# Kernel optimization log

Hardware: AMD Instinct MI355X
Metric: run time of the kernel (lower is better)

The kernel has to match this reference:

```python
import jax, jax.numpy as jnp
import numpy as np
import math

B, S, HID, NH, HD = 2, 1024, 768, 12, 64
MAXP = 1024  # max_position_embeddings


def setup_inputs() -> dict:
    key = jax.random.key(0)
    ks = jax.random.split(key, 12)
    s = 0.02
    return {
        "hidden_states": jax.random.normal(ks[0], (B, S, HID), jnp.float32),
        "attention_mask": jnp.zeros((B, 1, 1, S), jnp.float32),
        "scaled_attention_mask": jax.random.uniform(ks[1], (1, 1, S, S), dtype=jnp.float32),
        "selector_outputs": jax.random.uniform(ks[2], (B, 1, S, 1), dtype=jnp.float32),
        "Wq": jax.random.normal(ks[3], (HID, HID), jnp.float32) * s,
        "bq": jnp.zeros((HID,), jnp.float32),
        "Wk": jax.random.normal(ks[4], (HID, HID), jnp.float32) * s,
        "bk": jnp.zeros((HID,), jnp.float32),
        "Wv": jax.random.normal(ks[5], (HID, HID), jnp.float32) * s,
        "bv": jnp.zeros((HID,), jnp.float32),
        "dist_emb": jax.random.normal(ks[6], (2 * MAXP - 1, HD), jnp.float32) * s,
    }


def _heads(x):
    # [B,S,HID] -> [B,NH,S,HD]
    return x.reshape(B, S, NH, HD).transpose(0, 2, 1, 3)


def reference(hidden_states, attention_mask, scaled_attention_mask, selector_outputs,
              Wq, bq, Wk, bk, Wv, bv, dist_emb):
    q = _heads(hidden_states @ Wq + bq)  # [B,NH,S,HD]
    k = _heads(hidden_states @ Wk + bk)
    v = _heads(hidden_states @ Wv + bv)

    scores = jnp.einsum('bhld,bhrd->bhlr', q, k)  # [B,NH,S,S]

    # relative_key positional bias
    pos = jnp.arange(S)
    dist_idx = pos[:, None] - pos[None, :] + (MAXP - 1)  # [S,S] in [0, 2*MAXP-2]
    pos_emb = dist_emb[dist_idx]  # [S,S,HD]
    scores = scores + jnp.einsum('bhld,lrd->bhlr', q, pos_emb)

    scores = scores / math.sqrt(HD)
    scores = scores + attention_mask  # additive mask (global branch)

    probs = jax.nn.softmax(scores, axis=-1)  # dropout prob = 0.0 -> identity
    context = jnp.einsum('bhlr,bhrd->bhld', probs, v)

    # local (selector-gated) branch; note: attention_mask added a second time,
    # faithful to the original code
    scores_l = scores * scaled_attention_mask + attention_mask
    probs_l = jax.nn.softmax(scores_l, axis=-1)
    local_context = jnp.einsum('bhlr,bhrd->bhld', probs_l, v)

    sel = selector_outputs  # [B,1,S,1]
    context = sel * local_context + (1.0 - sel) * context  # [B,NH,S,HD]

    # [B,NH,S,HD] -> [B,S,HID]
    return context.transpose(0, 2, 1, 3).reshape(B, S, HID)
```

## Files before the change

kernel.cpp:

```cpp
#include <hip/hip_runtime.h>
#include <hip/hip_bf16.h>
#include <math.h>

#define BB   2
#define SS   1024
#define HIDD 768
#define NHH  12
#define HDD  64

typedef float f32x4 __attribute__((ext_vector_type(4)));
typedef short bf8   __attribute__((ext_vector_type(8)));
typedef unsigned short u16;
typedef unsigned int u32;
typedef u16 u16x8 __attribute__((ext_vector_type(8)));
typedef u16 u16x4 __attribute__((ext_vector_type(4)));

__device__ __forceinline__ u16 f2bf(float x) {
  unsigned int u = __float_as_uint(x);
  u += 0x7fffu + ((u >> 16) & 1u);
  return (u16)(u >> 16);
}
__device__ __forceinline__ float bf2f(u16 x) {
  return __uint_as_float(((u32)x) << 16);
}

__device__ __forceinline__ bf8 ldfrag(const u16* t, int row, int kc) {
  return *(const bf8*)&t[row * 64 + (kc ^ ((row & 7) << 3))];
}

__global__ __launch_bounds__(256) void xconv_kernel(const float* __restrict__ X,
                                                    u16* __restrict__ Xb) {
  int i = (blockIdx.x * 256 + threadIdx.x) * 8;
  float4 a = *(const float4*)&X[i];
  float4 b = *(const float4*)&X[i + 4];
  u16x8 o;
  o[0] = f2bf(a.x); o[1] = f2bf(a.y); o[2] = f2bf(a.z); o[3] = f2bf(a.w);
  o[4] = f2bf(b.x); o[5] = f2bf(b.y); o[6] = f2bf(b.z); o[7] = f2bf(b.w);
  *(u16x8*)&Xb[i] = o;
}

__global__ __launch_bounds__(256) void wtconv_kernel(
    const float* __restrict__ Wq, const float* __restrict__ Wk,
    const float* __restrict__ Wv, u16* __restrict__ Wt) {
  const int zi = blockIdx.z;
  const float* __restrict__ W = (zi == 0) ? Wq : (zi == 1 ? Wk : Wv);
  const int n0 = blockIdx.x * 64;
  const int k0 = blockIdx.y * 64;
  __shared__ float t[64][65];
  const int tid = threadIdx.x;
  {
    const int kl = tid >> 4;
    const int nl = (tid & 15) * 4;
#pragma unroll
    for (int p = 0; p < 4; ++p) {
      float4 v = *(const float4*)&W[(size_t)(k0 + kl + 16 * p) * HIDD + n0 + nl];
      t[kl + 16 * p][nl + 0] = v.x;
      t[kl + 16 * p][nl + 1] = v.y;
      t[kl + 16 * p][nl + 2] = v.z;
      t[kl + 16 * p][nl + 3] = v.w;
    }
  }
  __syncthreads();
  {
    const int nl = tid >> 4;
    const int cl = (tid & 15) * 4;
#pragma unroll
    for (int p = 0; p < 4; ++p) {
      const int n = nl + 16 * p;
      u16x4 o;
      o[0] = f2bf(t[cl + 0][n]);
      o[1] = f2bf(t[cl + 1][n]);
      o[2] = f2bf(t[cl + 2][n]);
      o[3] = f2bf(t[cl + 3][n]);
      *(u16x4*)&Wt[(size_t)(zi * HIDD + n0 + n) * HIDD + k0 + cl] = o;
    }
  }
}

__global__ __launch_bounds__(256) void econv_kernel(const float* __restrict__ demb,
                                                    u16* __restrict__ eb) {
  int i = (blockIdx.x * 256 + threadIdx.x) * 8;
  if (i < 2047 * HDD) {
    float4 a = *(const float4*)&demb[i];
    float4 b = *(const float4*)&demb[i + 4];
    u16x8 o;
    o[0] = f2bf(a.x); o[1] = f2bf(a.y); o[2] = f2bf(a.z); o[3] = f2bf(a.w);
    o[4] = f2bf(b.x); o[5] = f2bf(b.y); o[6] = f2bf(b.z); o[7] = f2bf(b.w);
    *(u16x8*)&eb[i] = o;
  }
}

__global__ __launch_bounds__(256) void qkv_mfma_kernel(
    const u16* __restrict__ Xb,
    const u16* __restrict__ Wt,
    const float* __restrict__ bq, const float* __restrict__ bk,
    const float* __restrict__ bv,
    u16* __restrict__ qb, u16* __restrict__ kb, u16* __restrict__ vt) {
  const int bn = blockIdx.x;
  const int bm = blockIdx.y;
  const int zi = bn / 6;

  __shared__ u16 As[64 * 64];
  __shared__ u16 Bs[128 * 64];

  const int tid  = threadIdx.x;
  const int lane = tid & 63;
  const int w    = tid >> 6;
  const int g    = lane >> 4;
  const int ln   = lane & 15;
  const int wm   = (w >> 1) * 32;
  const int wn   = (w & 1) * 64;

  f32x4 acc[2][4] = {};

  const int srow = tid >> 3;
  const int scol = (tid & 7) * 8;
  const u16* Ag = Xb + (size_t)(bm * 64 + srow) * HIDD + scol;
  const u16* Bg = Wt + (size_t)(bn * 128 + srow) * HIDD + scol;

  for (int k0 = 0; k0 < HIDD; k0 += 64) {
    if (k0) __syncthreads();
#pragma unroll
    for (int p = 0; p < 2; ++p) {
      const int r = srow + 32 * p;
      const int sw = (r & 7) << 3;
      *(u16x8*)&As[r * 64 + (scol ^ sw)] =
          *(const u16x8*)&Ag[(size_t)(32 * p) * HIDD + k0];
    }
#pragma unroll
    for (int p = 0; p < 4; ++p) {
      const int r = srow + 32 * p;
      const int sw = (r & 7) << 3;
      *(u16x8*)&Bs[r * 64 + (scol ^ sw)] =
          *(const u16x8*)&Bg[(size_t)(32 * p) * HIDD + k0];
    }
    __syncthreads();

    bf8 af[2][2], bfr[4][2];
#pragma unroll
    for (int f = 0; f < 2; ++f)
#pragma unroll
      for (int kk = 0; kk < 2; ++kk)
        af[f][kk] = ldfrag(As, wm + 16 * f + ln, kk * 32 + g * 8);
#pragma unroll
    for (int f = 0; f < 4; ++f)
#pragma unroll
      for (int kk = 0; kk < 2; ++kk)
        bfr[f][kk] = ldfrag(Bs, wn + 16 * f + ln, kk * 32 + g * 8);
    if (zi < 2) {
#pragma unroll
      for (int mf = 0; mf < 2; ++mf)
#pragma unroll
        for (int nf = 0; nf < 4; ++nf)
#pragma unroll
          for (int kk = 0; kk < 2; ++kk)
            acc[mf][nf] = __builtin_amdgcn_mfma_f32_16x16x32_bf16(
                bfr[nf][kk], af[mf][kk], acc[mf][nf], 0, 0, 0);
    } else {
#pragma unroll
      for (int mf = 0; mf < 2; ++mf)
#pragma unroll
        for (int nf = 0; nf < 4; ++nf)
#pragma unroll
          for (int kk = 0; kk < 2; ++kk)
            acc[mf][nf] = __builtin_amdgcn_mfma_f32_16x16x32_bf16(
                af[mf][kk], bfr[nf][kk], acc[mf][nf], 0, 0, 0);
    }
  }

  const int mrow  = bm * 64 + wm;
  const int nbase = (bn % 6) * 128 + wn;
  const int h     = nbase >> 6;

  if (zi < 2) {
    const float* __restrict__ bias = zi ? bk : bq;
    u16* __restrict__ outp = zi ? kb : qb;
#pragma unroll
    for (int nf = 0; nf < 4; ++nf) {
      const int d0 = 16 * nf + 4 * g;
      float4 bi = *(const float4*)&bias[nbase + d0];
#pragma unroll
      for (int mf = 0; mf < 2; ++mf) {
        const int m = mrow + 16 * mf + ln;
        const int b = m >> 10, s = m & 1023;
        u16x4 o;
        o[0] = f2bf(acc[mf][nf][0] + bi.x);
        o[1] = f2bf(acc[mf][nf][1] + bi.y);
        o[2] = f2bf(acc[mf][nf][2] + bi.z);
        o[3] = f2bf(acc[mf][nf][3] + bi.w);
        *(u16x4*)&outp[(((size_t)(b * NHH + h)) * SS + s) * HDD + d0] = o;
      }
    }
  } else {
#pragma unroll
    for (int nf = 0; nf < 4; ++nf) {
      const int d = 16 * nf + ln;
      const float bi = bv[nbase + d];
#pragma unroll
      for (int mf = 0; mf < 2; ++mf) {
        const int m = mrow + 16 * mf + 4 * g;
        const int b = m >> 10, s = m & 1023;
        u16x4 o;
        o[0] = f2bf(acc[mf][nf][0] + bi);
        o[1] = f2bf(acc[mf][nf][1] + bi);
        o[2] = f2bf(acc[mf][nf][2] + bi);
        o[3] = f2bf(acc[mf][nf][3] + bi);
        *(u16x4*)&vt[(((size_t)(b * NHH + h)) * HDD + d) * SS + s] = o;
      }
    }
  }
}

__global__ __launch_bounds__(256, 3) void attn_kernel(
    const u16* __restrict__ qbg,
    const u16* __restrict__ kbg,
    const u16* __restrict__ vtg,
    const u16* __restrict__ eb,
    const float* __restrict__ am,
    const float* __restrict__ smask,
    const float* __restrict__ selp,
    float* __restrict__ out) {
  const int l0 = blockIdx.x * 32;
  const int h  = blockIdx.y;
  const int b  = blockIdx.z;
  const int bh = b * NHH + h;
  const size_t hoff = (size_t)bh * SS * HDD;

  __shared__ __align__(16) u16 smbuf[16384];
  __shared__ __align__(4)  u16 tbuf[4 * 80 * 17];

  const int tid  = threadIdx.x;
  const int lane = tid & 63;
  const int w    = tid >> 6;
  const int p    = w >> 1;
  const int wp   = w & 1;
  const int g    = lane >> 4;
  const int ln   = lane & 15;

  u16* ksw = smbuf + p * 4096;
  u16* vsw = smbuf + 8192 + p * 4096;
  u16* Tw  = tbuf + w * (80 * 17);

  bf8 qf[2];
  {
    const u16* qp = qbg + hoff + (size_t)(l0 + 16 * wp + ln) * HDD + g * 8;
    qf[0] = *(const bf8*)(qp);
    qf[1] = *(const bf8*)(qp + 32);
  }

  f32x4 acc1[4] = {}, acc2[4] = {};
  float m1 = -INFINITY, m2 = -INFINITY, sum1 = 0.f, sum2 = 0.f;

  const int tid128 = tid & 127;
  const int rr = tid128 >> 2;
  const int cc = (tid128 & 3) << 4;
  const int S0i = ((lane & 16) << 1) | ln;
  const int S1i = S0i + 16;
  const bool ghi = (lane & 32) != 0;

  for (int t = 0; t < 8; ++t) {
    const int r0 = 512 * p + 64 * t;
    __syncthreads();

    const int W0 = l0 + 16 * wp - r0 + 960;
    bf8 ef[5][2];
#pragma unroll
    for (int c5 = 0; c5 < 5; ++c5) {
      const int gr = min(W0 + 16 * c5 + ln, 2046);
      const u16* ep = eb + (size_t)gr * HDD + g * 8;
      ef[c5][0] = *(const bf8*)(ep);
      ef[c5][1] = *(const bf8*)(ep + 32);
    }
    f32x4 amv[4], smv[4];
#pragma unroll
    for (int ct = 0; ct < 4; ++ct) {
      amv[ct] = *(const f32x4*)&am[(b << 10) + r0 + 16 * ct + 4 * g];
      smv[ct] = *(const f32x4*)&smask[(size_t)(l0 + 16 * wp + ln) * SS +
                                      r0 + 16 * ct + 4 * g];
    }
    {
      const u16* kgp = kbg + hoff + (size_t)r0 * HDD;
      const u16* vgp = vtg + hoff + r0;
#pragma unroll
      for (int pp = 0; pp < 2; ++pp) {
        const int r = rr + 32 * pp;
        const int sw = (r & 7) << 3;
        u16x8 a0 = *(const u16x8*)&kgp[(size_t)r * HDD + cc];
        u16x8 a1 = *(const u16x8*)&kgp[(size_t)r * HDD + cc + 8];
        *(u16x8*)&ksw[r * 64 + (cc ^ sw)] = a0;
        *(u16x8*)&ksw[r * 64 + ((cc + 8) ^ sw)] = a1;
        u16x8 c0 = *(const u16x8*)&vgp[(size_t)r * SS + cc];
        u16x8 c1 = *(const u16x8*)&vgp[(size_t)r * SS + cc + 8];
        *(u16x8*)&vsw[r * 64 + (cc ^ sw)] = c0;
        *(u16x8*)&vsw[r * 64 + ((cc + 8) ^ sw)] = c1;
      }
    }
    __syncthreads();

    __builtin_amdgcn_s_setprio(1);
#pragma unroll
    for (int c5 = 0; c5 < 5; ++c5) {
      f32x4 x = {0.f, 0.f, 0.f, 0.f};
      x = __builtin_amdgcn_mfma_f32_16x16x32_bf16(ef[c5][0], qf[0], x, 0, 0, 0);
      x = __builtin_amdgcn_mfma_f32_16x16x32_bf16(ef[c5][1], qf[1], x, 0, 0, 0);
#pragma unroll
      for (int i = 0; i < 4; ++i)
        Tw[(16 * c5 + 4 * g + i) * 17 + ln] = f2bf(x[i]);
    }
    f32x4 sc[4];
#pragma unroll
    for (int ct = 0; ct < 4; ++ct) {
      f32x4 x = {0.f, 0.f, 0.f, 0.f};
#pragma unroll
      for (int kk = 0; kk < 2; ++kk)
        x = __builtin_amdgcn_mfma_f32_16x16x32_bf16(
            ldfrag(ksw, ct * 16 + ln, kk * 32 + g * 8), qf[kk], x, 0, 0, 0);
      sc[ct] = x;
    }
    __builtin_amdgcn_s_setprio(0);

    float s1r[4][4], s2r[4][4];
#pragma unroll
    for (int ct = 0; ct < 4; ++ct)
#pragma unroll
      for (int i = 0; i < 4; ++i) {
        const int e = ln + 63 - 16 * ct - 4 * g - i;
        const float tb = bf2f(Tw[e * 17 + ln]);
        const float s1 = (sc[ct][i] + tb) * 0.125f + amv[ct][i];
        s1r[ct][i] = s1;
        s2r[ct][i] = s1 * smv[ct][i] + amv[ct][i];
      }

    bf8 pa1[2], pa2[2];
    {
      float mx = s1r[0][0];
#pragma unroll
      for (int ct = 0; ct < 4; ++ct)
#pragma unroll
        for (int i = 0; i < 4; ++i) mx = fmaxf(mx, s1r[ct][i]);
      mx = fmaxf(mx, __shfl_xor(mx, 16, 64));
      mx = fmaxf(mx, __shfl_xor(mx, 32, 64));
      const float mn = fmaxf(m1, mx);
      const float scl = __expf(m1 - mn);
      m1 = mn;
      float rs = 0.f;
      u32 pk[4][2];
#pragma unroll
      for (int ct = 0; ct < 4; ++ct) {
        const float p0 = __expf(s1r[ct][0] - mn);
        const float p1 = __expf(s1r[ct][1] - mn);
        const float p2 = __expf(s1r[ct][2] - mn);
        const float p3 = __expf(s1r[ct][3] - mn);
        rs += (p0 + p1) + (p2 + p3);
        pk[ct][0] = (u32)f2bf(p0) | ((u32)f2bf(p1) << 16);
        pk[ct][1] = (u32)f2bf(p2) | ((u32)f2bf(p3) << 16);
      }
      rs += __shfl_xor(rs, 16, 64);
      rs += __shfl_xor(rs, 32, 64);
      sum1 = sum1 * scl + rs;
#pragma unroll
      for (int i = 0; i < 4; ++i) {
        const float s = __shfl(scl, (lane & 48) + 4 * g + i, 64);
#pragma unroll
        for (int dt = 0; dt < 4; ++dt) acc1[dt][i] *= s;
      }
#pragma unroll
      for (int kk = 0; kk < 2; ++kk) {
        union { u32 u[4]; bf8 v; } f;
        const int cA = 2 * kk, cB = 2 * kk + 1;
        u32 a, bb;
        a = (u32)__shfl((int)pk[cA][0], S0i, 64);
        bb = (u32)__shfl((int)pk[cB][0], S0i, 64);
        f.u[0] = ghi ? bb : a;
        a = (u32)__shfl((int)pk[cA][1], S0i, 64);
        bb = (u32)__shfl((int)pk[cB][1], S0i, 64);
        f.u[1] = ghi ? bb : a;
        a = (u32)__shfl((int)pk[cA][0], S1i, 64);
        bb = (u32)__shfl((int)pk[cB][0], S1i, 64);
        f.u[2] = ghi ? bb : a;
        a = (u32)__shfl((int)pk[cA][1], S1i, 64);
        bb = (u32)__shfl((int)pk[cB][1], S1i, 64);
        f.u[3] = ghi ? bb : a;
        pa1[kk] = f.v;
      }
    }
    {
      float mx = s2r[0][0];
#pragma unroll
      for (int ct = 0; ct < 4; ++ct)
#pragma unroll
        for (int i = 0; i < 4; ++i) mx = fmaxf(mx, s2r[ct][i]);
      mx = fmaxf(mx, __shfl_xor(mx, 16, 64));
      mx = fmaxf(mx, __shfl_xor(mx, 32, 64));
      const float mn = fmaxf(m2, mx);
      const float scl = __expf(m2 - mn);
      m2 = mn;
      float rs = 0.f;
      u32 pk[4][2];
#pragma unroll
      for (int ct = 0; ct < 4; ++ct) {
        const float p0 = __expf(s2r[ct][0] - mn);
        const float p1 = __expf(s2r[ct][1] - mn);
        const float p2 = __expf(s2r[ct][2] - mn);
        const float p3 = __expf(s2r[ct][3] - mn);
        rs += (p0 + p1) + (p2 + p3);
        pk[ct][0] = (u32)f2bf(p0) | ((u32)f2bf(p1) << 16);
        pk[ct][1] = (u32)f2bf(p2) | ((u32)f2bf(p3) << 16);
      }
      rs += __shfl_xor(rs, 16, 64);
      rs += __shfl_xor(rs, 32, 64);
      sum2 = sum2 * scl + rs;
#pragma unroll
      for (int i = 0; i < 4; ++i) {
        const float s = __shfl(scl, (lane & 48) + 4 * g + i, 64);
#pragma unroll
        for (int dt = 0; dt < 4; ++dt) acc2[dt][i] *= s;
      }
#pragma unroll
      for (int kk = 0; kk < 2; ++kk) {
        union { u32 u[4]; bf8 v; } f;
        const int cA = 2 * kk, cB = 2 * kk + 1;
        u32 a, bb;
        a = (u32)__shfl((int)pk[cA][0], S0i, 64);
        bb = (u32)__shfl((int)pk[cB][0], S0i, 64);
        f.u[0] = ghi ? bb : a;
        a = (u32)__shfl((int)pk[cA][1], S0i, 64);
        bb = (u32)__shfl((int)pk[cB][1], S0i, 64);
        f.u[1] = ghi ? bb : a;
        a = (u32)__shfl((int)pk[cA][0], S1i, 64);
        bb = (u32)__shfl((int)pk[cB][0], S1i, 64);
        f.u[2] = ghi ? bb : a;
        a = (u32)__shfl((int)pk[cA][1], S1i, 64);
        bb = (u32)__shfl((int)pk[cB][1], S1i, 64);
        f.u[3] = ghi ? bb : a;
        pa2[kk] = f.v;
      }
    }

    __builtin_amdgcn_s_setprio(1);
#pragma unroll
    for (int kk = 0; kk < 2; ++kk) {
#pragma unroll
      for (int dt = 0; dt < 4; ++dt) {
        bf8 vb = ldfrag(vsw, dt * 16 + ln, kk * 32 + g * 8);
        acc1[dt] = __builtin_amdgcn_mfma_f32_16x16x32_bf16(pa1[kk], vb, acc1[dt], 0, 0, 0);
        acc2[dt] = __builtin_amdgcn_mfma_f32_16x16x32_bf16(pa2[kk], vb, acc2[dt], 0, 0, 0);
      }
    }
    __builtin_amdgcn_s_setprio(0);
  }

  __syncthreads();
  float* scr = (float*)smbuf;
  if (p == 1) {
#pragma unroll
    for (int i = 0; i < 4; ++i) {
      const int row = 4 * g + i;
#pragma unroll
      for (int dt = 0; dt < 4; ++dt) {
        scr[wp * 1024 + row * 64 + dt * 16 + ln] = acc1[dt][i];
        scr[2048 + wp * 1024 + row * 64 + dt * 16 + ln] = acc2[dt][i];
      }
    }
    if (g == 0) {
      const int sb = 4096 + (wp * 16 + ln) * 4;
      scr[sb + 0] = m1;
      scr[sb + 1] = sum1;
      scr[sb + 2] = m2;
      scr[sb + 3] = sum2;
    }
  }
  __syncthreads();
  if (p == 0) {
    const int sb = 4096 + (wp * 16 + ln) * 4;
    const float mB1 = scr[sb + 0], sB1 = scr[sb + 1];
    const float mB2 = scr[sb + 2], sB2 = scr[sb + 3];
    const float M1 = fmaxf(m1, mB1);
    const float e1A = __expf(m1 - M1), e1B = __expf(mB1 - M1);
    const float inv1 = 1.f / (sum1 * e1A + sB1 * e1B);
    const float a1 = e1A * inv1, c1 = e1B * inv1;
    const float M2 = fmaxf(m2, mB2);
    const float e2A = __expf(m2 - M2), e2B = __expf(mB2 - M2);
    const float inv2 = 1.f / (sum2 * e2A + sB2 * e2B);
    const float a2 = e2A * inv2, c2 = e2B * inv2;
#pragma unroll
    for (int i = 0; i < 4; ++i) {
      const int src = (lane & 48) + 4 * g + i;
      const float a1s = __shfl(a1, src, 64), c1s = __shfl(c1, src, 64);
      const float a2s = __shfl(a2, src, 64), c2s = __shfl(c2, src, 64);
      const int row = 4 * g + i;
      const int lg = l0 + 16 * wp + row;
      const float se = selp[(b << 10) + lg];
#pragma unroll
      for (int dt = 0; dt < 4; ++dt) {
        const float aB1 = scr[wp * 1024 + row * 64 + dt * 16 + ln];
        const float aB2 = scr[2048 + wp * 1024 + row * 64 + dt * 16 + ln];
        const float o1 = acc1[dt][i] * a1s + aB1 * c1s;
        const float o2 = acc2[dt][i] * a2s + aB2 * c2s;
        out[((size_t)((b << 10) + lg)) * HIDD + h * HDD + dt * 16 + ln] =
            se * o2 + (1.f - se) * o1;
      }
    }
  }
}

extern "C" void kernel_launch(void* const* d_in, const int* in_sizes, int n_in,
                              void* d_out, int out_size, void* d_ws, size_t ws_size,
                              hipStream_t stream) {
  const float* hidden = (const float*)d_in[0];
  const float* am     = (const float*)d_in[1];
  const float* smask  = (const float*)d_in[2];
  const float* selp   = (const float*)d_in[3];
  const float* Wq     = (const float*)d_in[4];
  const float* bq     = (const float*)d_in[5];
  const float* Wk     = (const float*)d_in[6];
  const float* bk     = (const float*)d_in[7];
  const float* Wv     = (const float*)d_in[8];
  const float* bv     = (const float*)d_in[9];
  const float* demb   = (const float*)d_in[10];
  float* out = (float*)d_out;

  u16* wsp = (u16*)d_ws;
  const size_t NEL = (size_t)BB * NHH * SS * HDD;
  u16* Xb  = wsp;
  u16* Wt  = Xb + (size_t)2048 * HIDD;
  u16* qbw = Wt + (size_t)3 * HIDD * HIDD;
  u16* kbw = qbw + NEL;
  u16* vtw = kbw + NEL;
  u16* ebw = vtw + NEL;

  xconv_kernel<<<768, 256, 0, stream>>>(hidden, Xb);
  dim3 gw(HIDD / 64, HIDD / 64, 3);
  wtconv_kernel<<<gw, 256, 0, stream>>>(Wq, Wk, Wv, Wt);
  econv_kernel<<<64, 256, 0, stream>>>(demb, ebw);

  dim3 g1(18, 32);
  qkv_mfma_kernel<<<g1, 256, 0, stream>>>(Xb, Wt, bq, bk, bv, qbw, kbw, vtw);

  dim3 g2(SS / 32, NHH, BB);
  attn_kernel<<<g2, 256, 0, stream>>>(qbw, kbw, vtw, ebw, am, smask, selp, out);
}
```

Before: 102.0 us.

## Load K/V fragments directly from global memory, drop LDS staging, remap blocks per XCD

New measurement: 138.7 us. 36.0% more time.

```diff
diff --git a/kernel.cpp b/kernel.cpp
--- a/kernel.cpp
+++ b/kernel.cpp
@@ -211,7 +211,7 @@
   }
 }
 
-__global__ __launch_bounds__(256, 3) void attn_kernel(
+__global__ __launch_bounds__(128, 3) void attn_kernel(
     const u16* __restrict__ qbg,
     const u16* __restrict__ kbg,
     const u16* __restrict__ vtg,
@@ -220,30 +220,33 @@
     const float* __restrict__ smask,
     const float* __restrict__ selp,
     float* __restrict__ out) {
-  const int l0 = blockIdx.x * 32;
-  const int h  = blockIdx.y;
-  const int b  = blockIdx.z;
+  const int d    = blockIdx.x;
+  const int xcd  = d & 7;
+  const int qq   = d >> 3;
+  const int inner = qq & 63;
+  const int grp  = qq >> 6;
+  const int hg   = grp * 8 + xcd;
+  const int h    = hg % NHH;
+  const int b    = hg / NHH;
+  const int l0   = inner * 16;
+
   const int bh = b * NHH + h;
   const size_t hoff = (size_t)bh * SS * HDD;
 
-  __shared__ __align__(16) u16 smbuf[16384];
-  __shared__ __align__(4)  u16 tbuf[4 * 80 * 17];
+  __shared__ __align__(4)  u16  tbuf[2 * 80 * 20];
+  __shared__ __align__(16) float scr[2112];
 
   const int tid  = threadIdx.x;
   const int lane = tid & 63;
   const int w    = tid >> 6;
-  const int p    = w >> 1;
-  const int wp   = w & 1;
   const int g    = lane >> 4;
   const int ln   = lane & 15;
 
-  u16* ksw = smbuf + p * 4096;
-  u16* vsw = smbuf + 8192 + p * 4096;
-  u16* Tw  = tbuf + w * (80 * 17);
+  u16* Tw = tbuf + w * (80 * 20);
 
   bf8 qf[2];
   {
-    const u16* qp = qbg + hoff + (size_t)(l0 + 16 * wp + ln) * HDD + g * 8;
+    const u16* qp = qbg + hoff + (size_t)(l0 + ln) * HDD + g * 8;
     qf[0] = *(const bf8*)(qp);
     qf[1] = *(const bf8*)(qp + 32);
   }
@@ -251,18 +254,21 @@
   f32x4 acc1[4] = {}, acc2[4] = {};
   float m1 = -INFINITY, m2 = -INFINITY, sum1 = 0.f, sum2 = 0.f;
 
-  const int tid128 = tid & 127;
-  const int rr = tid128 >> 2;
-  const int cc = (tid128 & 3) << 4;
   const int S0i = ((lane & 16) << 1) | ln;
   const int S1i = S0i + 16;
   const bool ghi = (lane & 32) != 0;
 
   for (int t = 0; t < 8; ++t) {
-    const int r0 = 512 * p + 64 * t;
-    __syncthreads();
-
-    const int W0 = l0 + 16 * wp - r0 + 960;
+    const int r0 = 512 * w + 64 * t;
+
+    bf8 kf[4][2];
+#pragma unroll
+    for (int ct = 0; ct < 4; ++ct) {
+      const u16* kp = kbg + hoff + (size_t)(r0 + 16 * ct + ln) * HDD + g * 8;
+      kf[ct][0] = *(const bf8*)(kp);
+      kf[ct][1] = *(const bf8*)(kp + 32);
+    }
+    const int W0 = l0 - r0 + 960;
     bf8 ef[5][2];
 #pragma unroll
     for (int c5 = 0; c5 < 5; ++c5) {
@@ -275,27 +281,8 @@
 #pragma unroll
     for (int ct = 0; ct < 4; ++ct) {
       amv[ct] = *(const f32x4*)&am[(b << 10) + r0 + 16 * ct + 4 * g];
-      smv[ct] = *(const f32x4*)&smask[(size_t)(l0 + 16 * wp + ln) * SS +
-                                      r0 + 16 * ct + 4 * g];
-    }
-    {
-      const u16* kgp = kbg + hoff + (size_t)r0 * HDD;
-      const u16* vgp = vtg + hoff + r0;
-#pragma unroll
-      for (int pp = 0; pp < 2; ++pp) {
-        const int r = rr + 32 * pp;
-        const int sw = (r & 7) << 3;
-        u16x8 a0 = *(const u16x8*)&kgp[(size_t)r * HDD + cc];
-        u16x8 a1 = *(const u16x8*)&kgp[(size_t)r * HDD + cc + 8];
-        *(u16x8*)&ksw[r * 64 + (cc ^ sw)] = a0;
-        *(u16x8*)&ksw[r * 64 + ((cc + 8) ^ sw)] = a1;
-        u16x8 c0 = *(const u16x8*)&vgp[(size_t)r * SS + cc];
-        u16x8 c1 = *(const u16x8*)&vgp[(size_t)r * SS + cc + 8];
-        *(u16x8*)&vsw[r * 64 + (cc ^ sw)] = c0;
-        *(u16x8*)&vsw[r * 64 + ((cc + 8) ^ sw)] = c1;
-      }
-    }
-    __syncthreads();
+      smv[ct] = *(const f32x4*)&smask[(size_t)(l0 + ln) * SS + r0 + 16 * ct + 4 * g];
+    }
 
     __builtin_amdgcn_s_setprio(1);
 #pragma unroll
@@ -305,16 +292,14 @@
       x = __builtin_amdgcn_mfma_f32_16x16x32_bf16(ef[c5][1], qf[1], x, 0, 0, 0);
 #pragma unroll
       for (int i = 0; i < 4; ++i)
-        Tw[(16 * c5 + 4 * g + i) * 17 + ln] = f2bf(x[i]);
+        Tw[(16 * c5 + 4 * g + i) * 20 + ln] = f2bf(x[i]);
     }
     f32x4 sc[4];
 #pragma unroll
     for (int ct = 0; ct < 4; ++ct) {
       f32x4 x = {0.f, 0.f, 0.f, 0.f};
-#pragma unroll
-      for (int kk = 0; kk < 2; ++kk)
-        x = __builtin_amdgcn_mfma_f32_16x16x32_bf16(
-            ldfrag(ksw, ct * 16 + ln, kk * 32 + g * 8), qf[kk], x, 0, 0, 0);
+      x = __builtin_amdgcn_mfma_f32_16x16x32_bf16(kf[ct][0], qf[0], x, 0, 0, 0);
+      x = __builtin_amdgcn_mfma_f32_16x16x32_bf16(kf[ct][1], qf[1], x, 0, 0, 0);
       sc[ct] = x;
     }
     __builtin_amdgcn_s_setprio(0);
@@ -325,7 +310,7 @@
 #pragma unroll
       for (int i = 0; i < 4; ++i) {
         const int e = ln + 63 - 16 * ct - 4 * g - i;
-        const float tb = bf2f(Tw[e * 17 + ln]);
+        const float tb = bf2f(Tw[e * 20 + ln]);
         const float s1 = (sc[ct][i] + tb) * 0.125f + amv[ct][i];
         s1r[ct][i] = s1;
         s2r[ct][i] = s1 * smv[ct][i] + amv[ct][i];
@@ -442,7 +427,8 @@
     for (int kk = 0; kk < 2; ++kk) {
 #pragma unroll
       for (int dt = 0; dt < 4; ++dt) {
-        bf8 vb = ldfrag(vsw, dt * 16 + ln, kk * 32 + g * 8);
+        const bf8 vb = *(const bf8*)(vtg + hoff + (size_t)(16 * dt + ln) * SS +
+                                     r0 + kk * 32 + g * 8);
         acc1[dt] = __builtin_amdgcn_mfma_f32_16x16x32_bf16(pa1[kk], vb, acc1[dt], 0, 0, 0);
         acc2[dt] = __builtin_amdgcn_mfma_f32_16x16x32_bf16(pa2[kk], vb, acc2[dt], 0, 0, 0);
       }
@@ -451,19 +437,18 @@
   }
 
   __syncthreads();
-  float* scr = (float*)smbuf;
-  if (p == 1) {
+  if (w == 1) {
 #pragma unroll
     for (int i = 0; i < 4; ++i) {
       const int row = 4 * g + i;
 #pragma unroll
       for (int dt = 0; dt < 4; ++dt) {
-        scr[wp * 1024 + row * 64 + dt * 16 + ln] = acc1[dt][i];
-        scr[2048 + wp * 1024 + row * 64 + dt * 16 + ln] = acc2[dt][i];
+        scr[row * 64 + dt * 16 + ln] = acc1[dt][i];
+        scr[1024 + row * 64 + dt * 16 + ln] = acc2[dt][i];
       }
     }
     if (g == 0) {
-      const int sb = 4096 + (wp * 16 + ln) * 4;
+      const int sb = 2048 + ln * 4;
       scr[sb + 0] = m1;
       scr[sb + 1] = sum1;
       scr[sb + 2] = m2;
@@ -471,8 +456,8 @@
     }
   }
   __syncthreads();
-  if (p == 0) {
-    const int sb = 4096 + (wp * 16 + ln) * 4;
+  if (w == 0) {
+    const int sb = 2048 + ln * 4;
     const float mB1 = scr[sb + 0], sB1 = scr[sb + 1];
     const float mB2 = scr[sb + 2], sB2 = scr[sb + 3];
     const float M1 = fmaxf(m1, mB1);
@@ -489,12 +474,12 @@
       const float a1s = __shfl(a1, src, 64), c1s = __shfl(c1, src, 64);
       const float a2s = __shfl(a2, src, 64), c2s = __shfl(c2, src, 64);
       const int row = 4 * g + i;
-      const int lg = l0 + 16 * wp + row;
+      const int lg = l0 + row;
       const float se = selp[(b << 10) + lg];
 #pragma unroll
       for (int dt = 0; dt < 4; ++dt) {
-        const float aB1 = scr[wp * 1024 + row * 64 + dt * 16 + ln];
-        const float aB2 = scr[2048 + wp * 1024 + row * 64 + dt * 16 + ln];
+        const float aB1 = scr[row * 64 + dt * 16 + ln];
+        const float aB2 = scr[1024 + row * 64 + dt * 16 + ln];
         const float o1 = acc1[dt][i] * a1s + aB1 * c1s;
         const float o2 = acc2[dt][i] * a2s + aB2 * c2s;
         out[((size_t)((b << 10) + lg)) * HIDD + h * HDD + dt * 16 + ln] =
@@ -537,6 +522,5 @@
   dim3 g1(18, 32);
   qkv_mfma_kernel<<<g1, 256, 0, stream>>>(Xb, Wt, bq, bk, bv, qbw, kbw, vtw);
 
-  dim3 g2(SS / 32, NHH, BB);
-  attn_kernel<<<g2, 256, 0, stream>>>(qbw, kbw, vtw, ebw, am, smask, selp, out);
-}
+  attn_kernel<<<1536, 128, 0, stream>>>(qbw, kbw, vtw, ebw, am, smask, selp, out);
+}
```

## Prefetch K/V tiles into registers, bf16 scaled mask, XCD-aware block remap

Applied to the files above, without the earlier changes.

Result: slower. 105.5 us (+3.5%).

```diff
diff --git a/kernel.cpp b/kernel.cpp
--- a/kernel.cpp
+++ b/kernel.cpp
@@ -90,6 +90,17 @@
   }
 }
 
+__global__ __launch_bounds__(256) void sconv_kernel(const float* __restrict__ sm,
+                                                    u16* __restrict__ smb) {
+  int i = (blockIdx.x * 256 + threadIdx.x) * 8;
+  float4 a = *(const float4*)&sm[i];
+  float4 b = *(const float4*)&sm[i + 4];
+  u16x8 o;
+  o[0] = f2bf(a.x); o[1] = f2bf(a.y); o[2] = f2bf(a.z); o[3] = f2bf(a.w);
+  o[4] = f2bf(b.x); o[5] = f2bf(b.y); o[6] = f2bf(b.z); o[7] = f2bf(b.w);
+  *(u16x8*)&smb[i] = o;
+}
+
 __global__ __launch_bounds__(256) void qkv_mfma_kernel(
     const u16* __restrict__ Xb,
     const u16* __restrict__ Wt,
@@ -217,17 +228,24 @@
     const u16* __restrict__ vtg,
     const u16* __restrict__ eb,
     const float* __restrict__ am,
-    const float* __restrict__ smask,
+    const u16* __restrict__ smb,
     const float* __restrict__ selp,
     float* __restrict__ out) {
-  const int l0 = blockIdx.x * 32;
-  const int h  = blockIdx.y;
-  const int b  = blockIdx.z;
+  const int bid  = blockIdx.x;
+  const int xcd  = bid & 7;
+  const int idx  = bid >> 3;
+  const int inner = idx & 31;
+  const int grp  = idx >> 5;
+  const int hg   = grp * 8 + xcd;
+  const int h    = hg % NHH;
+  const int b    = hg / NHH;
+  const int l0   = inner * 32;
+
   const int bh = b * NHH + h;
   const size_t hoff = (size_t)bh * SS * HDD;
 
   __shared__ __align__(16) u16 smbuf[16384];
-  __shared__ __align__(4)  u16 tbuf[4 * 80 * 17];
+  __shared__ __align__(4)  u16 tbuf[4 * 80 * 20];
 
   const int tid  = threadIdx.x;
   const int lane = tid & 63;
@@ -239,7 +257,7 @@
 
   u16* ksw = smbuf + p * 4096;
   u16* vsw = smbuf + 8192 + p * 4096;
-  u16* Tw  = tbuf + w * (80 * 17);
+  u16* Tw  = tbuf + w * (80 * 20);
 
   bf8 qf[2];
   {
@@ -258,9 +276,24 @@
   const int S1i = S0i + 16;
   const bool ghi = (lane & 32) != 0;
 
+  const u16* kgp0 = kbg + hoff;
+  const u16* vgp0 = vtg + hoff;
+
+  u16x8 kr[2][2], vr[2][2];
+  {
+    const int r0 = 512 * p;
+#pragma unroll
+    for (int pp = 0; pp < 2; ++pp) {
+      const int r = rr + 32 * pp;
+      kr[pp][0] = *(const u16x8*)&kgp0[(size_t)(r0 + r) * HDD + cc];
+      kr[pp][1] = *(const u16x8*)&kgp0[(size_t)(r0 + r) * HDD + cc + 8];
+      vr[pp][0] = *(const u16x8*)&vgp0[(size_t)r * SS + r0 + cc];
+      vr[pp][1] = *(const u16x8*)&vgp0[(size_t)r * SS + r0 + cc + 8];
+    }
+  }
+
   for (int t = 0; t < 8; ++t) {
     const int r0 = 512 * p + 64 * t;
-    __syncthreads();
 
     const int W0 = l0 + 16 * wp - r0 + 960;
     bf8 ef[5][2];
@@ -271,31 +304,38 @@
       ef[c5][0] = *(const bf8*)(ep);
       ef[c5][1] = *(const bf8*)(ep + 32);
     }
-    f32x4 amv[4], smv[4];
+    f32x4 amv[4];
+    u16x4 smv[4];
 #pragma unroll
     for (int ct = 0; ct < 4; ++ct) {
       amv[ct] = *(const f32x4*)&am[(b << 10) + r0 + 16 * ct + 4 * g];
-      smv[ct] = *(const f32x4*)&smask[(size_t)(l0 + 16 * wp + ln) * SS +
-                                      r0 + 16 * ct + 4 * g];
-    }
-    {
-      const u16* kgp = kbg + hoff + (size_t)r0 * HDD;
-      const u16* vgp = vtg + hoff + r0;
+      smv[ct] = *(const u16x4*)&smb[(size_t)(l0 + 16 * wp + ln) * SS +
+                                    r0 + 16 * ct + 4 * g];
+    }
+
+    __syncthreads();
+#pragma unroll
+    for (int pp = 0; pp < 2; ++pp) {
+      const int r = rr + 32 * pp;
+      const int sw = (r & 7) << 3;
+      *(u16x8*)&ksw[r * 64 + (cc ^ sw)] = kr[pp][0];
+      *(u16x8*)&ksw[r * 64 + ((cc + 8) ^ sw)] = kr[pp][1];
+      *(u16x8*)&vsw[r * 64 + (cc ^ sw)] = vr[pp][0];
+      *(u16x8*)&vsw[r * 64 + ((cc + 8) ^ sw)] = vr[pp][1];
+    }
+    __syncthreads();
+
+    if (t < 7) {
+      const int rn = r0 + 64;
 #pragma unroll
       for (int pp = 0; pp < 2; ++pp) {
         const int r = rr + 32 * pp;
-        const int sw = (r & 7) << 3;
-        u16x8 a0 = *(const u16x8*)&kgp[(size_t)r * HDD + cc];
-        u16x8 a1 = *(const u16x8*)&kgp[(size_t)r * HDD + cc + 8];
-        *(u16x8*)&ksw[r * 64 + (cc ^ sw)] = a0;
-        *(u16x8*)&ksw[r * 64 + ((cc + 8) ^ sw)] = a1;
-        u16x8 c0 = *(const u16x8*)&vgp[(size_t)r * SS + cc];
-        u16x8 c1 = *(const u16x8*)&vgp[(size_t)r * SS + cc + 8];
-        *(u16x8*)&vsw[r * 64 + (cc ^ sw)] = c0;
-        *(u16x8*)&vsw[r * 64 + ((cc + 8) ^ sw)] = c1;
-      }
-    }
-    __syncthreads();
+        kr[pp][0] = *(const u16x8*)&kgp0[(size_t)(rn + r) * HDD + cc];
+        kr[pp][1] = *(const u16x8*)&kgp0[(size_t)(rn + r) * HDD + cc + 8];
+        vr[pp][0] = *(const u16x8*)&vgp0[(size_t)r * SS + rn + cc];
+        vr[pp][1] = *(const u16x8*)&vgp0[(size_t)r * SS + rn + cc + 8];
+      }
+    }
 
     __builtin_amdgcn_s_setprio(1);
 #pragma unroll
@@ -305,7 +345,7 @@
       x = __builtin_amdgcn_mfma_f32_16x16x32_bf16(ef[c5][1], qf[1], x, 0, 0, 0);
 #pragma unroll
       for (int i = 0; i < 4; ++i)
-        Tw[(16 * c5 + 4 * g + i) * 17 + ln] = f2bf(x[i]);
+        Tw[(16 * c5 + 4 * g + i) * 20 + ln] = f2bf(x[i]);
     }
     f32x4 sc[4];
 #pragma unroll
@@ -325,10 +365,10 @@
 #pragma unroll
       for (int i = 0; i < 4; ++i) {
         const int e = ln + 63 - 16 * ct - 4 * g - i;
-        const float tb = bf2f(Tw[e * 17 + ln]);
+        const float tb = bf2f(Tw[e * 20 + ln]);
         const float s1 = (sc[ct][i] + tb) * 0.125f + amv[ct][i];
         s1r[ct][i] = s1;
-        s2r[ct][i] = s1 * smv[ct][i] + amv[ct][i];
+        s2r[ct][i] = s1 * bf2f(smv[ct][i]) + amv[ct][i];
       }
 
     bf8 pa1[2], pa2[2];
@@ -528,15 +568,16 @@
   u16* kbw = qbw + NEL;
   u16* vtw = kbw + NEL;
   u16* ebw = vtw + NEL;
+  u16* smb = ebw + (size_t)2047 * HDD;
 
   xconv_kernel<<<768, 256, 0, stream>>>(hidden, Xb);
   dim3 gw(HIDD / 64, HIDD / 64, 3);
   wtconv_kernel<<<gw, 256, 0, stream>>>(Wq, Wk, Wv, Wt);
   econv_kernel<<<64, 256, 0, stream>>>(demb, ebw);
+  sconv_kernel<<<512, 256, 0, stream>>>(smask, smb);
 
   dim3 g1(18, 32);
   qkv_mfma_kernel<<<g1, 256, 0, stream>>>(Xb, Wt, bq, bk, bv, qbw, kbw, vtw);
 
-  dim3 g2(SS / 32, NHH, BB);
-  attn_kernel<<<g2, 256, 0, stream>>>(qbw, kbw, vtw, ebw, am, smask, selp, out);
-}
+  attn_kernel<<<768, 256, 0, stream>>>(qbw, kbw, vtw, ebw, am, smb, selp, out);
+}
```
